# Kernel optimization log

Hardware: AMD Instinct MI355X
Metric: run time of the kernel (lower is better)

The kernel has to match this reference:

```python
import jax, jax.numpy as jnp
import numpy as np

# model hyperparameters (from init_kwargs 'model' mapping)
SIG = 10.0       # kernel length scale
C = 0.0          # energy integration constant
STD = 1.0        # normalization std
M, N_ATOMS = 64, 24
T_ROWS, DESC = 6000, N_ATOMS * (N_ATOMS - 1) // 2  # 276


def setup_inputs() -> dict:
    key = jax.random.key(0)
    k1, k2, k3 = jax.random.split(key, 3)
    # spread atoms out so pairwise distances are O(1..10) Angstrom-like
    Rs = jax.random.normal(k1, (M, N_ATOMS, 3), jnp.float32) * 3.0
    # training descriptors are inverse distances -> positive values in (0,1)
    xs_train = jax.random.uniform(k2, (T_ROWS, DESC), jnp.float32)
    Jx_alphas = jax.random.normal(k3, (T_ROWS, DESC), jnp.float32) * 0.1
    return {"Rs": Rs, "xs_train": xs_train, "Jx_alphas": Jx_alphas}


def reference(Rs, xs_train, Jx_alphas):
    sig = SIG
    q = np.sqrt(5.0) / sig
    m, n = Rs.shape[0], Rs.shape[1]
    i, j = np.tril_indices(n, k=-1)  # lower-triangular atom pairs, P entries

    # pairwise coordinate differences [M, N, N, 3]
    diffs = Rs[:, :, None, :] - Rs[:, None, :, :]
    # inverse pairwise distances over tril pairs -> descriptor xs [M, P]
    d_ij = jnp.linalg.norm(diffs[:, i, j, :], axis=-1)
    xs = 1.0 / d_ij

    # descriptor differences to all (permuted) training points [M, T, P]
    x_diffs = q * xs[:, None, :] - q * xs_train[None, :, :]
    x_dists = jnp.linalg.norm(x_diffs, axis=-1)            # [M, T]
    exp_xs = (5.0 / (3.0 * sig ** 2)) * jnp.exp(-x_dists)  # [M, T]
    dot = jnp.einsum('mtp,tp->mt', x_diffs, Jx_alphas)     # [M, T]
    exp1 = exp_xs * (1.0 + x_dists)                        # [M, T]

    F1 = jnp.einsum('mt,mtp->mp', exp_xs * dot, x_diffs)   # [M, P]
    F2 = exp1 @ Jx_alphas                                  # [M, P]
    Fs_x = (F1 - F2) * xs ** 3                             # [M, P]

    # scatter pair forces back onto the symmetric [N, N] pair grid;
    # diagonal diffs are zero so leaving mult=0 there matches the original
    mult = jnp.zeros((m, n, n), Rs.dtype)
    mult = mult.at[:, i, j].set(Fs_x).at[:, j, i].set(Fs_x)
    Fs = (diffs * mult[..., None]).sum(axis=1) * STD       # [M, N, 3]

    Es = (exp1 * dot).sum(axis=-1) / q * STD + C           # [M]
    return Es, Fs
```

## Files before the change

kernel.cpp:

```cpp
#include <hip/hip_runtime.h>
#include <math.h>

#define MM 64
#define NA 24
#define NP 276
#define NT 6000
#define QC 0.22360679774997896f
#define EXPC 0.01666666666666667f

#define G2S   56
#define G2R   108

#define OFF_WT   0
#define OFF_ET   387072
#define OFF_SLAB 774144
#define OFF_ESP  2752512
#define OFF_SWP  2776512
#define OFF_XS2  2800512
#define OFF_UU   2818176
#define OFF_VV   2818240
#define OFF_C1   2824240
#define OFF_F    2830240
#define SLABSTRIDE 35328

__device__ __forceinline__ void p2ij(int p, int& i, int& j) {
  int ii = (int)((1.0f + sqrtf(1.0f + 8.0f * (float)p)) * 0.5f);
  while (ii * (ii - 1) / 2 > p) ii--;
  while ((ii + 1) * ii / 2 <= p) ii++;
  j = p - ii * (ii - 1) / 2;
  i = ii;
}

__global__ __launch_bounds__(256) void k_pre(const float* __restrict__ Rs,
                                             const float* __restrict__ xt,
                                             const float* __restrict__ Ja,
                                             float* __restrict__ ws) {
  const int tid = threadIdx.x;
  const int bid = blockIdx.x;
  if (bid < MM) {
    if (bid < 2) {
      float* tz = ws + (bid ? OFF_ET : OFF_WT) + (size_t)NT * 64;
      for (int z = tid; z < 48 * 64; z += 256) tz[z] = 0.f;
    }
    const int m = bid;
    __shared__ float sR[NA * 3];
    __shared__ float sAcc[4];
    if (tid < NA * 3) sR[tid] = Rs[m * NA * 3 + tid];
    __syncthreads();
    float acc = 0.f;
    for (int p = tid; p < NP; p += 256) {
      int i, j;
      p2ij(p, i, j);
      const float dx = sR[i * 3 + 0] - sR[j * 3 + 0];
      const float dy = sR[i * 3 + 1] - sR[j * 3 + 1];
      const float dz = sR[i * 3 + 2] - sR[j * 3 + 2];
      const float u = 1.0f / sqrtf(dx * dx + dy * dy + dz * dz);
      ws[OFF_XS2 + (size_t)(m >> 5) * NP * 32 + p * 32 + (m & 31)] = u;
      acc = fmaf(u, u, acc);
    }
#pragma unroll
    for (int off = 32; off; off >>= 1) acc += __shfl_down(acc, off);
    if ((tid & 63) == 0) sAcc[tid >> 6] = acc;
    __syncthreads();
    if (tid == 0) ws[OFF_UU + m] = sAcc[0] + sAcc[1] + sAcc[2] + sAcc[3];
  } else {
    const int sb = bid - MM;
    const int t = sb * 4 + (tid >> 6);
    const int lane = tid & 63;
    const float* xr = xt + (size_t)t * NP;
    const float* jr = Ja + (size_t)t * NP;
    float a = 0.f, b = 0.f;
#pragma unroll
    for (int q = 0; q < 4; q++) {
      const float v = xr[lane + 64 * q];
      const float jj = jr[lane + 64 * q];
      a = fmaf(v, v, a);
      b = fmaf(v, jj, b);
    }
    if (lane < NP - 256) {
      const float v = xr[256 + lane];
      const float jj = jr[256 + lane];
      a = fmaf(v, v, a);
      b = fmaf(v, jj, b);
    }
#pragma unroll
    for (int off = 32; off; off >>= 1) {
      a += __shfl_down(a, off);
      b += __shfl_down(b, off);
    }
    if (lane == 0) { ws[OFF_VV + t] = a; ws[OFF_C1 + t] = b; }
  }
}

__global__ __launch_bounds__(256, 2) void k1(const float* __restrict__ xt,
                                             const float* __restrict__ Ja,
                                             float* __restrict__ ws) {
  __shared__ __align__(16) float Bv[16 * NP];
  __shared__ __align__(16) float Bj[16 * NP];
  __shared__ __align__(16) float As[NP * 32];
  __shared__ float sEsW[4][32], sSwW[4][32];
  const int tid = threadIdx.x;
  const int t0 = blockIdx.x * 16;
  const int m0 = blockIdx.y * 32;
  const int r = tid & 15;
  const int c = tid >> 4;

  const float vvt = ws[OFF_VV + t0 + c];
  const float c1t = ws[OFF_C1 + t0 + c];
  const float2 uu2 = *(const float2*)(ws + OFF_UU + m0 + 2 * r);

  {
    const float4* xs4 = (const float4*)(xt + (size_t)t0 * NP);
    const float4* js4 = (const float4*)(Ja + (size_t)t0 * NP);
    const float4* as4 = (const float4*)(ws + OFF_XS2 + (size_t)blockIdx.y * NP * 32);
    float4* bv4 = (float4*)Bv;
    float4* bj4 = (float4*)Bj;
    float4* a4  = (float4*)As;
    for (int i = tid; i < 16 * NP / 4; i += 256) { bv4[i] = xs4[i]; bj4[i] = js4[i]; }
    for (int i = tid; i < NP * 32 / 4; i += 256) a4[i] = as4[i];
  }
  __syncthreads();

  float av0 = 0.f, av1 = 0.f, aj0 = 0.f, aj1 = 0.f;
  const float* BvR = Bv + c * NP;
  const float* BjR = Bj + c * NP;
  const float* Ac = As + 2 * r;
#pragma unroll 3
  for (int kk = 0; kk < NP; kk += 4) {
    const float4 bv = *(const float4*)(BvR + kk);
    const float4 bj = *(const float4*)(BjR + kk);
    const float2 a0 = *(const float2*)(Ac + (kk + 0) * 32);
    const float2 a1 = *(const float2*)(Ac + (kk + 1) * 32);
    const float2 a2 = *(const float2*)(Ac + (kk + 2) * 32);
    const float2 a3 = *(const float2*)(Ac + (kk + 3) * 32);
    av0 = fmaf(a0.x, bv.x, av0); aj0 = fmaf(a0.x, bj.x, aj0);
    av1 = fmaf(a0.y, bv.x, av1); aj1 = fmaf(a0.y, bj.x, aj1);
    av0 = fmaf(a1.x, bv.y, av0); aj0 = fmaf(a1.x, bj.y, aj0);
    av1 = fmaf(a1.y, bv.y, av1); aj1 = fmaf(a1.y, bj.y, aj1);
    av0 = fmaf(a2.x, bv.z, av0); aj0 = fmaf(a2.x, bj.z, aj0);
    av1 = fmaf(a2.y, bv.z, av1); aj1 = fmaf(a2.y, bj.z, aj1);
    av0 = fmaf(a3.x, bv.w, av0); aj0 = fmaf(a3.x, bj.w, aj0);
    av1 = fmaf(a3.y, bv.w, av1); aj1 = fmaf(a3.y, bj.w, aj1);
  }

  float es2[2], sw2[2], wv[2], ev[2];
#pragma unroll
  for (int i = 0; i < 2; i++) {
    const float g1v = i ? av1 : av0;
    const float g2v = i ? aj1 : aj0;
    const float uum = i ? uu2.y : uu2.x;
    float d2 = fmaxf(uum - 2.f * g1v + vvt, 0.f);
    float xd = QC * sqrtf(d2);
    float dv = QC * (g2v - c1t);
    float ex = EXPC * __expf(-xd);
    float e1v = ex * (1.f + xd);
    float w_ = ex * dv;
    wv[i] = w_; ev[i] = e1v;
    es2[i] = e1v * dv;
    sw2[i] = w_;
  }
  const int t = t0 + c;
  *(float2*)(ws + OFF_WT + (size_t)t * 64 + m0 + 2 * r) = make_float2(wv[0], wv[1]);
  *(float2*)(ws + OFF_ET + (size_t)t * 64 + m0 + 2 * r) = make_float2(ev[0], ev[1]);

#pragma unroll
  for (int i = 0; i < 2; i++) {
    es2[i] += __shfl_down(es2[i], 32); es2[i] += __shfl_down(es2[i], 16);
    sw2[i] += __shfl_down(sw2[i], 32); sw2[i] += __shfl_down(sw2[i], 16);
  }
  const int w = tid >> 6;
  if ((tid & 63) < 16) {
    sEsW[w][2 * r + 0] = es2[0]; sEsW[w][2 * r + 1] = es2[1];
    sSwW[w][2 * r + 0] = sw2[0]; sSwW[w][2 * r + 1] = sw2[1];
  }
  __syncthreads();
  if (tid < 32) {
    const float es = sEsW[0][tid] + sEsW[1][tid] + sEsW[2][tid] + sEsW[3][tid];
    const float sw = sSwW[0][tid] + sSwW[1][tid] + sSwW[2][tid] + sSwW[3][tid];
    ws[OFF_ESP + (size_t)blockIdx.x * 64 + m0 + tid] = es;
    ws[OFF_SWP + (size_t)blockIdx.x * 64 + m0 + tid] = sw;
  }
}

__global__ __launch_bounds__(256, 2) void k2(const float* __restrict__ xt,
                                             const float* __restrict__ Ja,
                                             float* __restrict__ ws) {
  __shared__ __align__(16) float Aw[G2R * 64];
  __shared__ __align__(16) float Ae[G2R * 64];
  __shared__ __align__(16) float2 Bvj[G2R][18];
  const int tid = threadIdx.x;
  const int p0 = blockIdx.x * 16;
  const int cid = blockIdx.y;
  const int k0 = cid * G2R;
  const int validp = (NP - p0 < 16) ? (NP - p0) : 16;
  const int r = tid & 31;
  const int c = tid >> 5;

  {
    const float4* aws = (const float4*)(ws + OFF_WT + (size_t)k0 * 64);
    const float4* aes = (const float4*)(ws + OFF_ET + (size_t)k0 * 64);
    float4* aw4 = (float4*)Aw;
    float4* ae4 = (float4*)Ae;
    for (int idx = tid; idx < G2R * 16; idx += 256) { aw4[idx] = aws[idx]; ae4[idx] = aes[idx]; }
  }
  for (int idx = tid; idx < G2R * 4; idx += 256) {
    const int k = idx >> 2;
    const int pq = (idx & 3) * 4;
    const int t = k0 + k;
    float4 v = make_float4(0.f, 0.f, 0.f, 0.f), j = v;
    if (pq < validp && t < NT) {
      v = *(const float4*)(xt + (size_t)t * NP + p0 + pq);
      j = *(const float4*)(Ja + (size_t)t * NP + p0 + pq);
    }
    *(float4*)&Bvj[k][pq]     = make_float4(v.x, j.x, v.y, j.y);
    *(float4*)&Bvj[k][pq + 2] = make_float4(v.z, j.z, v.w, j.w);
  }
  __syncthreads();

  float f1[2][2] = {{0.f, 0.f}, {0.f, 0.f}};
  float f2[2][2] = {{0.f, 0.f}, {0.f, 0.f}};
#pragma unroll 4
  for (int k = 0; k < G2R; k++) {
    const float2 aw = *(const float2*)&Aw[k * 64 + 2 * r];
    const float2 ae = *(const float2*)&Ae[k * 64 + 2 * r];
    const float4 b  = *(const float4*)&Bvj[k][2 * c];
    f1[0][0] = fmaf(aw.x, b.x, f1[0][0]); f1[0][1] = fmaf(aw.x, b.z, f1[0][1]);
    f1[1][0] = fmaf(aw.y, b.x, f1[1][0]); f1[1][1] = fmaf(aw.y, b.z, f1[1][1]);
    f2[0][0] = fmaf(ae.x, b.y, f2[0][0]); f2[0][1] = fmaf(ae.x, b.w, f2[0][1]);
    f2[1][0] = fmaf(ae.y, b.y, f2[1][0]); f2[1][1] = fmaf(ae.y, b.w, f2[1][1]);
  }

#pragma unroll
  for (int j = 0; j < 2; j++) {
    const int pl = 2 * c + j;
    if (pl < validp) {
      const int p = p0 + pl;
      float* b1 = ws + OFF_SLAB + ((size_t)(cid * 2 + 0) * NP + p) * 64;
      float* b2 = ws + OFF_SLAB + ((size_t)(cid * 2 + 1) * NP + p) * 64;
      *(float2*)(b1 + 2 * r) = make_float2(f1[0][j], f1[1][j]);
      *(float2*)(b2 + 2 * r) = make_float2(f2[0][j], f2[1][j]);
    }
  }
}

__global__ __launch_bounds__(128) void k_red(float* __restrict__ ws) {
  const int inner = blockIdx.x * 128 + threadIdx.x;
  const float* src = ws + OFF_SLAB + inner;
  float s = 0.f;
#pragma unroll
  for (int cid = 0; cid < G2S; cid++) s += src[(size_t)cid * SLABSTRIDE];
  ws[OFF_F + inner] = s;
}

__global__ __launch_bounds__(320) void k3(const float* __restrict__ Rs,
                                          const float* __restrict__ ws,
                                          float* __restrict__ out) {
  const int m = blockIdx.x;
  const int tid = threadIdx.x;
  __shared__ float fx[NP];
  __shared__ float sR[NA * 3];
  __shared__ float sEsw[5], sSww[5];
  __shared__ float sTot[2];
  if (tid < NA * 3) sR[tid] = Rs[m * NA * 3 + tid];

  float aE = 0.f, aS = 0.f;
  for (int tt = tid; tt < 375; tt += 320) {
    aE += ws[OFF_ESP + (size_t)tt * 64 + m];
    aS += ws[OFF_SWP + (size_t)tt * 64 + m];
  }
#pragma unroll
  for (int off = 32; off; off >>= 1) {
    aE += __shfl_down(aE, off);
    aS += __shfl_down(aS, off);
  }
  if ((tid & 63) == 0) { sEsw[tid >> 6] = aE; sSww[tid >> 6] = aS; }
  __syncthreads();
  if (tid == 0) {
    float e = 0.f, s = 0.f;
#pragma unroll
    for (int w = 0; w < 5; w++) { e += sEsw[w]; s += sSww[w]; }
    sTot[0] = e; sTot[1] = s;
    out[m] = e / QC;
  }
  __syncthreads();
  const float sw = sTot[1];

  for (int p = tid; p < NP; p += 320) {
    const float f1p = ws[OFF_F + (size_t)0 * NP * 64 + p * 64 + m];
    const float f2  = ws[OFF_F + (size_t)1 * NP * 64 + p * 64 + m];
    const float u = ws[OFF_XS2 + (size_t)(m >> 5) * NP * 32 + p * 32 + (m & 31)];
    const float F1 = QC * (u * sw - f1p);
    fx[p] = (F1 - f2) * u * u * u;
  }
  __syncthreads();

  if (tid < NA * 3) {
    const int a = tid / 3, cc = tid % 3;
    const float ra = sR[a * 3 + cc];
    float acc = 0.f;
    for (int b = 0; b < NA; b++) {
      if (b == a) continue;
      const int i = a > b ? a : b, j = a > b ? b : a;
      const int p = i * (i - 1) / 2 + j;
      acc += (sR[b * 3 + cc] - ra) * fx[p];
    }
    out[MM + m * NA * 3 + tid] = acc;
  }
}

extern "C" void kernel_launch(void* const* d_in, const int* in_sizes, int n_in,
                              void* d_out, int out_size, void* d_ws, size_t ws_size,
                              hipStream_t stream) {
  const float* Rs = (const float*)d_in[0];
  const float* xt = (const float*)d_in[1];
  const float* Ja = (const float*)d_in[2];
  float* out = (float*)d_out;
  float* ws = (float*)d_ws;

  k_pre<<<MM + 1500, 256, 0, stream>>>(Rs, xt, Ja, ws);
  k1<<<dim3(375, 2), 256, 0, stream>>>(xt, Ja, ws);
  k2<<<dim3(18, G2S), 256, 0, stream>>>(xt, Ja, ws);
  k_red<<<NP * 2, 128, 0, stream>>>(ws);
  k3<<<MM, 320, 0, stream>>>(Rs, ws, out);
}
```

Measured before the change: 118.2 us.

## Use larger register tiles with split-K across warps in k1 and k2

Both GEMM-like kernels now give each thread a larger register tile: 4 m by 2 t in k1, and 4 m by 4 p in k2. The K dimension is split across the four wavefronts, and the partial sums are then combined through shared memory by wavefront 0. This raises arithmetic intensity per shared-memory load and cuts LDS traffic. In exchange it adds an extra reduction pass and sync, more register pressure, and epilogue work serialized onto one wavefront.

```diff
diff --git a/kernel.cpp b/kernel.cpp
--- a/kernel.cpp
+++ b/kernel.cpp
@@ -92,22 +92,33 @@
   }
 }
 
+#define K1SUB(A, vb0, vb1, jb0, jb1)                                               \
+  av0[0] = fmaf(A.x, vb0, av0[0]); av0[1] = fmaf(A.y, vb0, av0[1]);                \
+  av0[2] = fmaf(A.z, vb0, av0[2]); av0[3] = fmaf(A.w, vb0, av0[3]);                \
+  av1[0] = fmaf(A.x, vb1, av1[0]); av1[1] = fmaf(A.y, vb1, av1[1]);                \
+  av1[2] = fmaf(A.z, vb1, av1[2]); av1[3] = fmaf(A.w, vb1, av1[3]);                \
+  aj0[0] = fmaf(A.x, jb0, aj0[0]); aj0[1] = fmaf(A.y, jb0, aj0[1]);                \
+  aj0[2] = fmaf(A.z, jb0, aj0[2]); aj0[3] = fmaf(A.w, jb0, aj0[3]);                \
+  aj1[0] = fmaf(A.x, jb1, aj1[0]); aj1[1] = fmaf(A.y, jb1, aj1[1]);                \
+  aj1[2] = fmaf(A.z, jb1, aj1[2]); aj1[3] = fmaf(A.w, jb1, aj1[3]);
+
 __global__ __launch_bounds__(256, 2) void k1(const float* __restrict__ xt,
                                              const float* __restrict__ Ja,
                                              float* __restrict__ ws) {
   __shared__ __align__(16) float Bv[16 * NP];
   __shared__ __align__(16) float Bj[16 * NP];
   __shared__ __align__(16) float As[NP * 32];
-  __shared__ float sEsW[4][32], sSwW[4][32];
   const int tid = threadIdx.x;
   const int t0 = blockIdx.x * 16;
   const int m0 = blockIdx.y * 32;
-  const int r = tid & 15;
-  const int c = tid >> 4;
-
-  const float vvt = ws[OFF_VV + t0 + c];
-  const float c1t = ws[OFF_C1 + t0 + c];
-  const float2 uu2 = *(const float2*)(ws + OFF_UU + m0 + 2 * r);
+  const int w = tid >> 6;
+  const int lane = tid & 63;
+  const int mg = lane & 7;
+  const int tg = lane >> 3;
+
+  const float4 uu4 = *(const float4*)(ws + OFF_UU + m0 + 4 * mg);
+  const float2 vv2 = *(const float2*)(ws + OFF_VV + t0 + 2 * tg);
+  const float2 c12 = *(const float2*)(ws + OFF_C1 + t0 + 2 * tg);
 
   {
     const float4* xs4 = (const float4*)(xt + (size_t)t0 * NP);
@@ -121,64 +132,90 @@
   }
   __syncthreads();
 
-  float av0 = 0.f, av1 = 0.f, aj0 = 0.f, aj1 = 0.f;
-  const float* BvR = Bv + c * NP;
-  const float* BjR = Bj + c * NP;
-  const float* Ac = As + 2 * r;
-#pragma unroll 3
-  for (int kk = 0; kk < NP; kk += 4) {
-    const float4 bv = *(const float4*)(BvR + kk);
-    const float4 bj = *(const float4*)(BjR + kk);
-    const float2 a0 = *(const float2*)(Ac + (kk + 0) * 32);
-    const float2 a1 = *(const float2*)(Ac + (kk + 1) * 32);
-    const float2 a2 = *(const float2*)(Ac + (kk + 2) * 32);
-    const float2 a3 = *(const float2*)(Ac + (kk + 3) * 32);
-    av0 = fmaf(a0.x, bv.x, av0); aj0 = fmaf(a0.x, bj.x, aj0);
-    av1 = fmaf(a0.y, bv.x, av1); aj1 = fmaf(a0.y, bj.x, aj1);
-    av0 = fmaf(a1.x, bv.y, av0); aj0 = fmaf(a1.x, bj.y, aj0);
-    av1 = fmaf(a1.y, bv.y, av1); aj1 = fmaf(a1.y, bj.y, aj1);
-    av0 = fmaf(a2.x, bv.z, av0); aj0 = fmaf(a2.x, bj.z, aj0);
-    av1 = fmaf(a2.y, bv.z, av1); aj1 = fmaf(a2.y, bj.z, aj1);
-    av0 = fmaf(a3.x, bv.w, av0); aj0 = fmaf(a3.x, bj.w, aj0);
-    av1 = fmaf(a3.y, bv.w, av1); aj1 = fmaf(a3.y, bj.w, aj1);
-  }
-
-  float es2[2], sw2[2], wv[2], ev[2];
-#pragma unroll
-  for (int i = 0; i < 2; i++) {
-    const float g1v = i ? av1 : av0;
-    const float g2v = i ? aj1 : aj0;
-    const float uum = i ? uu2.y : uu2.x;
-    float d2 = fmaxf(uum - 2.f * g1v + vvt, 0.f);
-    float xd = QC * sqrtf(d2);
-    float dv = QC * (g2v - c1t);
-    float ex = EXPC * __expf(-xd);
-    float e1v = ex * (1.f + xd);
-    float w_ = ex * dv;
-    wv[i] = w_; ev[i] = e1v;
-    es2[i] = e1v * dv;
-    sw2[i] = w_;
-  }
-  const int t = t0 + c;
-  *(float2*)(ws + OFF_WT + (size_t)t * 64 + m0 + 2 * r) = make_float2(wv[0], wv[1]);
-  *(float2*)(ws + OFF_ET + (size_t)t * 64 + m0 + 2 * r) = make_float2(ev[0], ev[1]);
-
-#pragma unroll
-  for (int i = 0; i < 2; i++) {
-    es2[i] += __shfl_down(es2[i], 32); es2[i] += __shfl_down(es2[i], 16);
-    sw2[i] += __shfl_down(sw2[i], 32); sw2[i] += __shfl_down(sw2[i], 16);
-  }
-  const int w = tid >> 6;
-  if ((tid & 63) < 16) {
-    sEsW[w][2 * r + 0] = es2[0]; sEsW[w][2 * r + 1] = es2[1];
-    sSwW[w][2 * r + 0] = sw2[0]; sSwW[w][2 * r + 1] = sw2[1];
-  }
-  __syncthreads();
-  if (tid < 32) {
-    const float es = sEsW[0][tid] + sEsW[1][tid] + sEsW[2][tid] + sEsW[3][tid];
-    const float sw = sSwW[0][tid] + sSwW[1][tid] + sSwW[2][tid] + sSwW[3][tid];
-    ws[OFF_ESP + (size_t)blockIdx.x * 64 + m0 + tid] = es;
-    ws[OFF_SWP + (size_t)blockIdx.x * 64 + m0 + tid] = sw;
+  float av0[4] = {0.f, 0.f, 0.f, 0.f}, av1[4] = {0.f, 0.f, 0.f, 0.f};
+  float aj0[4] = {0.f, 0.f, 0.f, 0.f}, aj1[4] = {0.f, 0.f, 0.f, 0.f};
+  const float* BvR0 = Bv + (2 * tg + 0) * NP;
+  const float* BvR1 = Bv + (2 * tg + 1) * NP;
+  const float* BjR0 = Bj + (2 * tg + 0) * NP;
+  const float* BjR1 = Bj + (2 * tg + 1) * NP;
+  const float* Ac = As + 4 * mg;
+  const int kbeg = w * 68;
+  const int kend = (w == 3) ? NP : (kbeg + 68);
+#pragma unroll 2
+  for (int k = kbeg; k < kend; k += 4) {
+    const float4 a0 = *(const float4*)(Ac + (k + 0) * 32);
+    const float4 a1 = *(const float4*)(Ac + (k + 1) * 32);
+    const float4 a2 = *(const float4*)(Ac + (k + 2) * 32);
+    const float4 a3 = *(const float4*)(Ac + (k + 3) * 32);
+    const float4 bv0 = *(const float4*)(BvR0 + k);
+    const float4 bv1 = *(const float4*)(BvR1 + k);
+    const float4 bj0 = *(const float4*)(BjR0 + k);
+    const float4 bj1 = *(const float4*)(BjR1 + k);
+    K1SUB(a0, bv0.x, bv1.x, bj0.x, bj1.x)
+    K1SUB(a1, bv0.y, bv1.y, bj0.y, bj1.y)
+    K1SUB(a2, bv0.z, bv1.z, bj0.z, bj1.z)
+    K1SUB(a3, bv0.w, bv1.w, bj0.w, bj1.w)
+  }
+  __syncthreads();
+
+  if (w > 0) {
+    float* red = As + (size_t)(w - 1) * 16 * 64;
+#pragma unroll
+    for (int q = 0; q < 4; q++) {
+      red[(q + 0) * 64 + lane]  = av0[q];
+      red[(q + 4) * 64 + lane]  = av1[q];
+      red[(q + 8) * 64 + lane]  = aj0[q];
+      red[(q + 12) * 64 + lane] = aj1[q];
+    }
+  }
+  __syncthreads();
+  if (w == 0) {
+#pragma unroll
+    for (int ww = 0; ww < 3; ww++) {
+      const float* red = As + (size_t)ww * 16 * 64;
+#pragma unroll
+      for (int q = 0; q < 4; q++) {
+        av0[q] += red[(q + 0) * 64 + lane];
+        av1[q] += red[(q + 4) * 64 + lane];
+        aj0[q] += red[(q + 8) * 64 + lane];
+        aj1[q] += red[(q + 12) * 64 + lane];
+      }
+    }
+    float es[4] = {0.f, 0.f, 0.f, 0.f}, swv[4] = {0.f, 0.f, 0.f, 0.f};
+    const float uum[4] = {uu4.x, uu4.y, uu4.z, uu4.w};
+#pragma unroll
+    for (int tj = 0; tj < 2; tj++) {
+      const float vvt = tj ? vv2.y : vv2.x;
+      const float c1t = tj ? c12.y : c12.x;
+      const float* g1 = tj ? av1 : av0;
+      const float* g2 = tj ? aj1 : aj0;
+      float wq[4], eq[4];
+#pragma unroll
+      for (int mi = 0; mi < 4; mi++) {
+        const float d2 = fmaxf(uum[mi] - 2.f * g1[mi] + vvt, 0.f);
+        const float xd = QC * sqrtf(d2);
+        const float dv = QC * (g2[mi] - c1t);
+        const float ex = EXPC * __expf(-xd);
+        const float e1v = ex * (1.f + xd);
+        const float w_ = ex * dv;
+        wq[mi] = w_; eq[mi] = e1v;
+        es[mi] += e1v * dv; swv[mi] += w_;
+      }
+      const int t = t0 + 2 * tg + tj;
+      *(float4*)(ws + OFF_WT + (size_t)t * 64 + m0 + 4 * mg) = make_float4(wq[0], wq[1], wq[2], wq[3]);
+      *(float4*)(ws + OFF_ET + (size_t)t * 64 + m0 + 4 * mg) = make_float4(eq[0], eq[1], eq[2], eq[3]);
+    }
+#pragma unroll
+    for (int q = 0; q < 4; q++) {
+      es[q] += __shfl_down(es[q], 32); es[q] += __shfl_down(es[q], 16); es[q] += __shfl_down(es[q], 8);
+      swv[q] += __shfl_down(swv[q], 32); swv[q] += __shfl_down(swv[q], 16); swv[q] += __shfl_down(swv[q], 8);
+    }
+    if (lane < 8) {
+      *(float4*)(ws + OFF_ESP + (size_t)blockIdx.x * 64 + m0 + 4 * lane) =
+          make_float4(es[0], es[1], es[2], es[3]);
+      *(float4*)(ws + OFF_SWP + (size_t)blockIdx.x * 64 + m0 + 4 * lane) =
+          make_float4(swv[0], swv[1], swv[2], swv[3]);
+    }
   }
 }
 
@@ -187,14 +224,16 @@
                                              float* __restrict__ ws) {
   __shared__ __align__(16) float Aw[G2R * 64];
   __shared__ __align__(16) float Ae[G2R * 64];
-  __shared__ __align__(16) float2 Bvj[G2R][18];
+  __shared__ __align__(16) float2 Bvj[G2R][16];
   const int tid = threadIdx.x;
   const int p0 = blockIdx.x * 16;
   const int cid = blockIdx.y;
   const int k0 = cid * G2R;
   const int validp = (NP - p0 < 16) ? (NP - p0) : 16;
-  const int r = tid & 31;
-  const int c = tid >> 5;
+  const int w = tid >> 6;
+  const int lane = tid & 63;
+  const int mg = lane & 15;
+  const int pg = lane >> 4;
 
   {
     const float4* aws = (const float4*)(ws + OFF_WT + (size_t)k0 * 64);
@@ -217,28 +256,66 @@
   }
   __syncthreads();
 
-  float f1[2][2] = {{0.f, 0.f}, {0.f, 0.f}};
-  float f2[2][2] = {{0.f, 0.f}, {0.f, 0.f}};
-#pragma unroll 4
-  for (int k = 0; k < G2R; k++) {
-    const float2 aw = *(const float2*)&Aw[k * 64 + 2 * r];
-    const float2 ae = *(const float2*)&Ae[k * 64 + 2 * r];
-    const float4 b  = *(const float4*)&Bvj[k][2 * c];
-    f1[0][0] = fmaf(aw.x, b.x, f1[0][0]); f1[0][1] = fmaf(aw.x, b.z, f1[0][1]);
-    f1[1][0] = fmaf(aw.y, b.x, f1[1][0]); f1[1][1] = fmaf(aw.y, b.z, f1[1][1]);
-    f2[0][0] = fmaf(ae.x, b.y, f2[0][0]); f2[0][1] = fmaf(ae.x, b.w, f2[0][1]);
-    f2[1][0] = fmaf(ae.y, b.y, f2[1][0]); f2[1][1] = fmaf(ae.y, b.w, f2[1][1]);
-  }
-
-#pragma unroll
-  for (int j = 0; j < 2; j++) {
-    const int pl = 2 * c + j;
-    if (pl < validp) {
-      const int p = p0 + pl;
-      float* b1 = ws + OFF_SLAB + ((size_t)(cid * 2 + 0) * NP + p) * 64;
-      float* b2 = ws + OFF_SLAB + ((size_t)(cid * 2 + 1) * NP + p) * 64;
-      *(float2*)(b1 + 2 * r) = make_float2(f1[0][j], f1[1][j]);
-      *(float2*)(b2 + 2 * r) = make_float2(f2[0][j], f2[1][j]);
+  float f1[4][4] = {{0.f}}, f2[4][4] = {{0.f}};
+  const float* AwL = Aw + 4 * mg;
+  const float* AeL = Ae + 4 * mg;
+  const int kb = w * 27;
+  const int ke = kb + 27;
+#pragma unroll 3
+  for (int k = kb; k < ke; ++k) {
+    const float4 aw = *(const float4*)(AwL + (size_t)k * 64);
+    const float4 ae = *(const float4*)(AeL + (size_t)k * 64);
+    const float4 b01 = *(const float4*)&Bvj[k][4 * pg];
+    const float4 b23 = *(const float4*)&Bvj[k][4 * pg + 2];
+    const float vb[4] = {b01.x, b01.z, b23.x, b23.z};
+    const float jb[4] = {b01.y, b01.w, b23.y, b23.w};
+    const float aww[4] = {aw.x, aw.y, aw.z, aw.w};
+    const float aee[4] = {ae.x, ae.y, ae.z, ae.w};
+#pragma unroll
+    for (int mi = 0; mi < 4; mi++)
+#pragma unroll
+      for (int pj = 0; pj < 4; pj++) {
+        f1[mi][pj] = fmaf(aww[mi], vb[pj], f1[mi][pj]);
+        f2[mi][pj] = fmaf(aee[mi], jb[pj], f2[mi][pj]);
+      }
+  }
+  __syncthreads();
+
+  if (w > 0) {
+    float* red = Aw + (size_t)(w - 1) * 32 * 64;
+#pragma unroll
+    for (int mi = 0; mi < 4; mi++)
+#pragma unroll
+      for (int pj = 0; pj < 4; pj++) {
+        red[(mi * 4 + pj) * 64 + lane]        = f1[mi][pj];
+        red[(16 + mi * 4 + pj) * 64 + lane]   = f2[mi][pj];
+      }
+  }
+  __syncthreads();
+  if (w == 0) {
+#pragma unroll
+    for (int ww = 0; ww < 3; ww++) {
+      const float* red = Aw + (size_t)ww * 32 * 64;
+#pragma unroll
+      for (int mi = 0; mi < 4; mi++)
+#pragma unroll
+        for (int pj = 0; pj < 4; pj++) {
+          f1[mi][pj] += red[(mi * 4 + pj) * 64 + lane];
+          f2[mi][pj] += red[(16 + mi * 4 + pj) * 64 + lane];
+        }
+    }
+    float* b1 = ws + OFF_SLAB + (size_t)(cid * 2 + 0) * NP * 64;
+    float* b2 = ws + OFF_SLAB + (size_t)(cid * 2 + 1) * NP * 64;
+#pragma unroll
+    for (int pj = 0; pj < 4; pj++) {
+      const int pl = 4 * pg + pj;
+      if (pl < validp) {
+        const int p = p0 + pl;
+        *(float4*)(b1 + (size_t)p * 64 + 4 * mg) =
+            make_float4(f1[0][pj], f1[1][pj], f1[2][pj], f1[3][pj]);
+        *(float4*)(b2 + (size_t)p * 64 + 4 * mg) =
+            make_float4(f2[0][pj], f2[1][pj], f2[2][pj], f2[3][pj]);
+      }
     }
   }
 }
```

Result: faster. 115.3 us (-2.5%).
